# Kernel optimization log

Measured on AMD Instinct MI355X. Metric: run time of the kernel, lower is better.

Reference implementation:

```python
import jax, jax.numpy as jnp
import numpy as np

DIM = 768
NUM_HEADS = 12
HEAD_DIM = DIM // NUM_HEADS
SCALE = HEAD_DIM ** -0.5


def setup_inputs() -> dict:
    key = jax.random.key(0)
    k1, k2, k3, k4 = jax.random.split(key, 4)
    B, N, C = 4, 2048, DIM
    x = jax.random.normal(k1, (B, N, C), dtype=jnp.float32)
    # nn.Linear(dim, 3*dim, bias=False): weight shape (3C, C), y = x @ W^T
    w_qkv = jax.random.normal(k2, (3 * C, C), dtype=jnp.float32) * (C ** -0.5)
    # nn.Linear(dim, dim) with default bias=True
    w_proj = jax.random.normal(k3, (C, C), dtype=jnp.float32) * (C ** -0.5)
    b_proj = jax.random.normal(k4, (C,), dtype=jnp.float32) * 0.02
    return {"x": x, "w_qkv": w_qkv, "w_proj": w_proj, "b_proj": b_proj}


def reference(x, w_qkv, w_proj, b_proj):
    B, N, C = x.shape
    H, D = NUM_HEADS, HEAD_DIM
    qkv = jnp.einsum('bnc,oc->bno', x, w_qkv)  # (B, N, 3C)
    qkv = qkv.reshape(B, N, 3, H, D).transpose(2, 0, 3, 1, 4)  # (3, B, H, N, D)
    q, k, v = qkv[0], qkv[1], qkv[2]
    attn = jnp.einsum('bhnd,bhmd->bhnm', q, k) * jnp.float32(SCALE)  # (B,H,N,N)
    attn = jax.nn.softmax(attn, axis=-1)
    out = jnp.einsum('bhnm,bhmd->bhnd', attn, v)  # (B,H,N,D)
    out = out.transpose(0, 2, 1, 3).reshape(B, N, C)
    out = jnp.einsum('bnc,oc->bno', out, w_proj) + b_proj
    return out
```

## Files before the change

kernel.cpp:

```cpp
#include <hip/hip_runtime.h>
#include <math.h>

#define B_ 4
#define N_ 2048
#define C_ 768
#define H_ 12
#define D_ 64
#define QKSCALE_ 0.18033688011112042f

typedef unsigned short u16;
typedef unsigned int u32;
typedef short s16x8 __attribute__((ext_vector_type(8)));
typedef float f32x4 __attribute__((ext_vector_type(4)));
typedef u32 u32x2 __attribute__((ext_vector_type(2)));

__device__ __forceinline__ u16 f2bf(float f) {
    union { float f; u32 u; } v; v.f = f;
    u32 r = (v.u + 0x7fffu + ((v.u >> 16) & 1u)) >> 16;
    return (u16)r;
}

#if __has_builtin(__builtin_amdgcn_cvt_pk_bf16_f32)
__device__ __forceinline__ u32 pkbf(float a, float b) {
    auto r = __builtin_amdgcn_cvt_pk_bf16_f32(a, b);
    u32 u; __builtin_memcpy(&u, &r, 4);
    return u;
}
#else
__device__ __forceinline__ u32 pkbf(float a, float b) {
    union { float f; u32 u; } ua, ub; ua.f = a; ub.f = b;
    u32 ra = ua.u + 0x7fffu + ((ua.u >> 16) & 1u);
    u32 rb = ub.u + 0x7fffu + ((ub.u >> 16) & 1u);
    return __builtin_amdgcn_perm(rb, ra, 0x07060302u);
}
#endif

__device__ __forceinline__ void gl_lds16(const u16* g, u16* l) {
    __builtin_amdgcn_global_load_lds(
        (__attribute__((address_space(1))) void*)g,
        (__attribute__((address_space(3))) void*)l, 16, 0, 0);
}

#define NX4_  (B_ * N_ * C_ / 4)
#define NWQ4_ (3 * C_ * C_ / 4)
#define NWP4_ (C_ * C_ / 4)
__global__ __launch_bounds__(256) void cvt_all(const float4* __restrict__ x,
                                               const float4* __restrict__ wq,
                                               const float4* __restrict__ wp,
                                               ushort4* __restrict__ xb,
                                               ushort4* __restrict__ wqb,
                                               ushort4* __restrict__ wpb)
{
    const int tot = NX4_ + NWQ4_ + NWP4_;
    int i = blockIdx.x * blockDim.x + threadIdx.x;
    const int stride = gridDim.x * blockDim.x;
    for (; i < tot; i += stride) {
        const float4* s; ushort4* d; int j;
        if (i < NX4_)              { s = x;  d = xb;  j = i; }
        else if (i < NX4_ + NWQ4_) { s = wq; d = wqb; j = i - NX4_; }
        else                       { s = wp; d = wpb; j = i - NX4_ - NWQ4_; }
        float4 v = s[j];
        ushort4 o;
        o.x = f2bf(v.x); o.y = f2bf(v.y); o.z = f2bf(v.z); o.w = f2bf(v.w);
        d[j] = o;
    }
}

template<int BM, bool OUT_BF16, bool BIAS, bool QSCALE>
__global__ __launch_bounds__(256) void gemm_mfma(const u16* __restrict__ A,
                                                 const u16* __restrict__ Bm,
                                                 const float* __restrict__ bias,
                                                 void* __restrict__ Cout,
                                                 int M, int N, int K)
{
    constexpr int MF = BM / 32;
    constexpr int ASZ = BM * 32, BSZ = 128 * 32;
    __shared__ __align__(16) u16 As[2 * ASZ];
    __shared__ __align__(16) u16 Bs[2 * BSZ];
    const int tid  = threadIdx.x;
    const int wv   = tid >> 6;
    const int lane = tid & 63;
    const int lr   = lane & 15;
    const int lq   = lane >> 4;
    const int wm   = (wv >> 1) * (BM / 2);
    const int wn   = (wv & 1) * 64;
    const int row0 = blockIdx.y * BM, col0 = blockIdx.x * 128;

    f32x4 acc[MF][4];
    #pragma unroll
    for (int i = 0; i < MF; i++)
        #pragma unroll
        for (int j = 0; j < 4; j++) { f32x4 z = {0.f,0.f,0.f,0.f}; acc[i][j] = z; }

    const int srow   = lane >> 2;
    const int schunk = (((lane & 3) ^ ((lane >> 3) & 3)) * 8);

    const int arow_base = (BM == 128) ? 32 * wv : 16 * wv;
    const u16* gA0 = A + (size_t)(row0 + arow_base + srow) * K + schunk;
    const u16* gA1 = gA0 + (size_t)16 * K;
    const u16* gB0 = Bm + (size_t)(col0 + 32 * wv + srow) * K + schunk;
    const u16* gB1 = gB0 + (size_t)16 * K;
    const int aoff0 = arow_base * 32, aoff1 = aoff0 + 16 * 32;
    const int boff0 = (32 * wv) * 32, boff1 = boff0 + 16 * 32;

    const int ppos = (lq ^ ((lr >> 1) & 3)) * 8;
    const int nIter = K / 32;

    gl_lds16(gA0, As + aoff0);
    if (BM == 128) gl_lds16(gA1, As + aoff1);
    gl_lds16(gB0, Bs + boff0);
    gl_lds16(gB1, Bs + boff1);

    for (int t = 0; t < nIter; t++) {
        const int cur = t & 1;
        __syncthreads();
        if (t + 1 < nIter) {
            const int k1 = (t + 1) * 32;
            const int nb = cur ^ 1;
            gl_lds16(gA0 + k1, As + nb * ASZ + aoff0);
            if (BM == 128) gl_lds16(gA1 + k1, As + nb * ASZ + aoff1);
            gl_lds16(gB0 + k1, Bs + nb * BSZ + boff0);
            gl_lds16(gB1 + k1, Bs + nb * BSZ + boff1);
        }
        const u16* __restrict__ Ac = As + cur * ASZ;
        const u16* __restrict__ Bc = Bs + cur * BSZ;
        s16x8 af[MF], bfr[4];
        #pragma unroll
        for (int i = 0; i < MF; i++)
            af[i] = *(const s16x8*)&Ac[(wm + 16*i + lr) * 32 + ppos];
        #pragma unroll
        for (int j = 0; j < 4; j++)
            bfr[j] = *(const s16x8*)&Bc[(wn + 16*j + lr) * 32 + ppos];
        #pragma unroll
        for (int i = 0; i < MF; i++)
            #pragma unroll
            for (int j = 0; j < 4; j++)
                acc[i][j] = __builtin_amdgcn_mfma_f32_16x16x32_bf16(af[i], bfr[j], acc[i][j], 0, 0, 0);
    }

    #pragma unroll
    for (int i = 0; i < MF; i++) {
        #pragma unroll
        for (int j = 0; j < 4; j++) {
            const int col = col0 + wn + 16*j + lr;
            float bv = BIAS ? bias[col] : 0.f;
            #pragma unroll
            for (int r = 0; r < 4; r++) {
                const int row = row0 + wm + 16*i + lq*4 + r;
                float v = acc[i][j][r] + bv;
                if (QSCALE && col < C_) v *= QKSCALE_;
                if (OUT_BF16) ((u16*)Cout)[(size_t)row * N + col] = f2bf(v);
                else          ((float*)Cout)[(size_t)row * N + col] = v;
            }
        }
    }
}

__global__ __launch_bounds__(256, 3) void attn_mfma(const u16* __restrict__ qkv,
                                                    u16* __restrict__ attout)
{
    __shared__ __align__(16) u16 Ks[64][72];
    __shared__ __align__(16) u16 Vt[64][72];
    __shared__ __align__(16) u16 Ps[128][72];

    const int tid  = threadIdx.x;
    const int wv   = tid >> 6;
    const int lane = tid & 63;
    const int lr   = lane & 15;
    const int lq   = lane >> 4;
    const int n0   = blockIdx.x * 128;
    const int bh   = blockIdx.y, b = bh / H_, h = bh % H_;
    const size_t rs = 3 * C_;

    const u16* Qg = qkv + ((size_t)b * N_ + n0) * rs + h * D_;
    const u16* Kg = qkv + ((size_t)b * N_) * rs + C_ + h * D_;
    const u16* Vg = Kg + C_;

    s16x8 qf[2][2];
    #pragma unroll
    for (int iq = 0; iq < 2; iq++)
        #pragma unroll
        for (int kk = 0; kk < 2; kk++)
            qf[iq][kk] = *(const s16x8*)(Qg + (size_t)(32*wv + 16*iq + lr) * rs + kk*32 + lq*8);

    f32x4 oacc[2][4];
    float li[2] = {0.f, 0.f};
    #pragma unroll
    for (int i = 0; i < 2; i++)
        #pragma unroll
        for (int j = 0; j < 4; j++) { f32x4 z = {0.f,0.f,0.f,0.f}; oacc[i][j] = z; }

    const int skey = tid >> 2, sd0 = (tid & 3) * 16;
    const int vc = tid & 7, vp = tid >> 3;
    const int vkey0 = 2 * vp, vd0 = vc * 8;
    const int vcol0 = (vkey0 + 8 * vc) & 63;

    s16x8 kr0, kr1, vr0, vr1;
    {
        const u16* kp = Kg + (size_t)skey * rs + sd0;
        kr0 = *(const s16x8*)kp; kr1 = *(const s16x8*)(kp + 8);
        const u16* vp2 = Vg + (size_t)vkey0 * rs + vd0;
        vr0 = *(const s16x8*)vp2; vr1 = *(const s16x8*)(vp2 + rs);
    }

    for (int t = 0; t < N_ / 64; t++) {
        __syncthreads();
        *(s16x8*)&Ks[skey][sd0]     = kr0;
        *(s16x8*)&Ks[skey][sd0 + 8] = kr1;
        #pragma unroll
        for (int u = 0; u < 8; u++) {
            u32 pk = (u32)(u16)vr0[u] | ((u32)(u16)vr1[u] << 16);
            *(u32*)&Vt[vd0 + u][vcol0] = pk;
        }
        __syncthreads();
        if (t + 1 < N_ / 64) {
            const u16* kp = Kg + (size_t)((t+1)*64 + skey) * rs + sd0;
            kr0 = *(const s16x8*)kp; kr1 = *(const s16x8*)(kp + 8);
            const u16* vp2 = Vg + (size_t)((t+1)*64 + vkey0) * rs + vd0;
            vr0 = *(const s16x8*)vp2; vr1 = *(const s16x8*)(vp2 + rs);
        }

        f32x4 st[4][2];
        #pragma unroll
        for (int jk = 0; jk < 4; jk++)
            #pragma unroll
            for (int iq = 0; iq < 2; iq++) { f32x4 z = {0.f,0.f,0.f,0.f}; st[jk][iq] = z; }
        #pragma unroll
        for (int kk = 0; kk < 2; kk++) {
            s16x8 kf[4];
            #pragma unroll
            for (int jk = 0; jk < 4; jk++)
                kf[jk] = *(const s16x8*)&Ks[16*jk + lr][kk*32 + lq*8];
            #pragma unroll
            for (int jk = 0; jk < 4; jk++) {
                st[jk][0] = __builtin_amdgcn_mfma_f32_16x16x32_bf16(kf[jk], qf[0][kk], st[jk][0], 0, 0, 0);
                st[jk][1] = __builtin_amdgcn_mfma_f32_16x16x32_bf16(kf[jk], qf[1][kk], st[jk][1], 0, 0, 0);
            }
        }

        #pragma unroll
        for (int jk = 0; jk < 4; jk++)
            #pragma unroll
            for (int iq = 0; iq < 2; iq++) {
                const float p0 = __builtin_amdgcn_exp2f(st[jk][iq][0]);
                const float p1 = __builtin_amdgcn_exp2f(st[jk][iq][1]);
                const float p2 = __builtin_amdgcn_exp2f(st[jk][iq][2]);
                const float p3 = __builtin_amdgcn_exp2f(st[jk][iq][3]);
                li[iq] += (p0 + p1) + (p2 + p3);
                u32x2 w;
                w.x = pkbf(p0, p1);
                w.y = pkbf(p2, p3);
                *(u32x2*)&Ps[32*wv + 16*iq + lr][16*jk + 4*lq] = w;
            }

        #pragma unroll
        for (int kk = 0; kk < 2; kk++) {
            s16x8 ap0 = *(const s16x8*)&Ps[32*wv      + lr][kk*32 + lq*8];
            s16x8 ap1 = *(const s16x8*)&Ps[32*wv + 16 + lr][kk*32 + lq*8];
            #pragma unroll
            for (int j2 = 0; j2 < 4; j2++) {
                const int pb = ((kk*4 + lq) + 2*j2 + (lr >> 3)) & 7;
                s16x8 bv = *(const s16x8*)&Vt[16*j2 + lr][pb * 8];
                oacc[0][j2] = __builtin_amdgcn_mfma_f32_16x16x32_bf16(ap0, bv, oacc[0][j2], 0, 0, 0);
                oacc[1][j2] = __builtin_amdgcn_mfma_f32_16x16x32_bf16(ap1, bv, oacc[1][j2], 0, 0, 0);
            }
        }
    }

    #pragma unroll
    for (int iq = 0; iq < 2; iq++) {
        li[iq] += __shfl_xor(li[iq], 16);
        li[iq] += __shfl_xor(li[iq], 32);
    }
    #pragma unroll
    for (int iq = 0; iq < 2; iq++) {
        #pragma unroll
        for (int r = 0; r < 4; r++) {
            const float inv = 1.f / __shfl(li[iq], 4*lq + r);
            const int row = n0 + 32*wv + 16*iq + 4*lq + r;
            #pragma unroll
            for (int j2 = 0; j2 < 4; j2++)
                attout[((size_t)(b * N_ + row)) * C_ + h * D_ + 16*j2 + lr] =
                    f2bf(oacc[iq][j2][r] * inv);
        }
    }
}

extern "C" void kernel_launch(void* const* d_in, const int* in_sizes, int n_in,
                              void* d_out, int out_size, void* d_ws, size_t ws_size,
                              hipStream_t stream) {
    const float* x      = (const float*)d_in[0];
    const float* w_qkv  = (const float*)d_in[1];
    const float* w_proj = (const float*)d_in[2];
    const float* b_proj = (const float*)d_in[3];
    float* out = (float*)d_out;

    const int NX   = B_ * N_ * C_;
    const int NWQ  = 3 * C_ * C_;
    const int NWP  = C_ * C_;
    const int NQKV = B_ * N_ * 3 * C_;

    u16* xb   = (u16*)d_ws;
    u16* wqb  = xb + NX;
    u16* wpb  = wqb + NWQ;
    u16* qkvb = wpb + NWP;
    u16* attb = qkvb + NQKV;

    dim3 blk(256);

    cvt_all<<<768, blk, 0, stream>>>((const float4*)x, (const float4*)w_qkv,
                                     (const float4*)w_proj,
                                     (ushort4*)xb, (ushort4*)wqb, (ushort4*)wpb);

    const int M = B_ * N_;
    gemm_mfma<128, true, false, true><<<dim3((3*C_)/128, M/128), blk, 0, stream>>>(
        xb, wqb, nullptr, qkvb, M, 3*C_, C_);

    attn_mfma<<<dim3(N_/128, B_ * H_), blk, 0, stream>>>(qkvb, attb);

    gemm_mfma<64, false, true, false><<<dim3(C_/128, M/64), blk, 0, stream>>>(
        attb, wpb, b_proj, out, M, C_, C_);
}
```

Before: 227.5 us.

## Enlarge QKV GEMM tile, swizzle attention LDS, raise occupancy bounds

New measurement: 241.8 us. +6.3%, slower.

```diff
diff --git a/kernel.cpp b/kernel.cpp
--- a/kernel.cpp
+++ b/kernel.cpp
@@ -20,20 +20,12 @@
     return (u16)r;
 }
 
-#if __has_builtin(__builtin_amdgcn_cvt_pk_bf16_f32)
-__device__ __forceinline__ u32 pkbf(float a, float b) {
-    auto r = __builtin_amdgcn_cvt_pk_bf16_f32(a, b);
-    u32 u; __builtin_memcpy(&u, &r, 4);
-    return u;
-}
-#else
 __device__ __forceinline__ u32 pkbf(float a, float b) {
     union { float f; u32 u; } ua, ub; ua.f = a; ub.f = b;
     u32 ra = ua.u + 0x7fffu + ((ua.u >> 16) & 1u);
     u32 rb = ub.u + 0x7fffu + ((ub.u >> 16) & 1u);
     return __builtin_amdgcn_perm(rb, ra, 0x07060302u);
 }
-#endif
 
 __device__ __forceinline__ void gl_lds16(const u16* g, u16* l) {
     __builtin_amdgcn_global_load_lds(
@@ -66,14 +58,15 @@
     }
 }
 
-template<int BM, bool OUT_BF16, bool BIAS, bool QSCALE>
-__global__ __launch_bounds__(256) void gemm_mfma(const u16* __restrict__ A,
-                                                 const u16* __restrict__ Bm,
-                                                 const float* __restrict__ bias,
-                                                 void* __restrict__ Cout,
-                                                 int M, int N, int K)
+template<int BM, int WPEU, bool OUT_BF16, bool BIAS, bool QSCALE>
+__global__ __launch_bounds__(256, WPEU) void gemm_mfma(const u16* __restrict__ A,
+                                                       const u16* __restrict__ Bm,
+                                                       const float* __restrict__ bias,
+                                                       void* __restrict__ Cout,
+                                                       int M, int N, int K)
 {
     constexpr int MF = BM / 32;
+    constexpr int ACALLS = BM / 64;
     constexpr int ASZ = BM * 32, BSZ = 128 * 32;
     __shared__ __align__(16) u16 As[2 * ASZ];
     __shared__ __align__(16) u16 Bs[2 * BSZ];
@@ -95,19 +88,19 @@
     const int srow   = lane >> 2;
     const int schunk = (((lane & 3) ^ ((lane >> 3) & 3)) * 8);
 
-    const int arow_base = (BM == 128) ? 32 * wv : 16 * wv;
+    const int arow_base = (BM / 4) * wv;
     const u16* gA0 = A + (size_t)(row0 + arow_base + srow) * K + schunk;
-    const u16* gA1 = gA0 + (size_t)16 * K;
     const u16* gB0 = Bm + (size_t)(col0 + 32 * wv + srow) * K + schunk;
     const u16* gB1 = gB0 + (size_t)16 * K;
-    const int aoff0 = arow_base * 32, aoff1 = aoff0 + 16 * 32;
+    const int aoff0 = arow_base * 32;
     const int boff0 = (32 * wv) * 32, boff1 = boff0 + 16 * 32;
 
     const int ppos = (lq ^ ((lr >> 1) & 3)) * 8;
     const int nIter = K / 32;
 
-    gl_lds16(gA0, As + aoff0);
-    if (BM == 128) gl_lds16(gA1, As + aoff1);
+    #pragma unroll
+    for (int c = 0; c < ACALLS; c++)
+        gl_lds16(gA0 + (size_t)(16 * c) * K, As + aoff0 + c * 16 * 32);
     gl_lds16(gB0, Bs + boff0);
     gl_lds16(gB1, Bs + boff1);
 
@@ -117,8 +110,10 @@
         if (t + 1 < nIter) {
             const int k1 = (t + 1) * 32;
             const int nb = cur ^ 1;
-            gl_lds16(gA0 + k1, As + nb * ASZ + aoff0);
-            if (BM == 128) gl_lds16(gA1 + k1, As + nb * ASZ + aoff1);
+            #pragma unroll
+            for (int c = 0; c < ACALLS; c++)
+                gl_lds16(gA0 + (size_t)(16 * c) * K + k1,
+                         As + nb * ASZ + aoff0 + c * 16 * 32);
             gl_lds16(gB0 + k1, Bs + nb * BSZ + boff0);
             gl_lds16(gB1 + k1, Bs + nb * BSZ + boff1);
         }
@@ -156,12 +151,12 @@
     }
 }
 
-__global__ __launch_bounds__(256, 3) void attn_mfma(const u16* __restrict__ qkv,
+__global__ __launch_bounds__(256, 4) void attn_mfma(const u16* __restrict__ qkv,
                                                     u16* __restrict__ attout)
 {
-    __shared__ __align__(16) u16 Ks[64][72];
+    __shared__ __align__(16) u16 Ks[64 * 64];
     __shared__ __align__(16) u16 Vt[64][72];
-    __shared__ __align__(16) u16 Ps[128][72];
+    __shared__ __align__(16) u16 Ps[128 * 64];
 
     const int tid  = threadIdx.x;
     const int wv   = tid >> 6;
@@ -190,14 +185,17 @@
         #pragma unroll
         for (int j = 0; j < 4; j++) { f32x4 z = {0.f,0.f,0.f,0.f}; oacc[i][j] = z; }
 
-    const int skey = tid >> 2, sd0 = (tid & 3) * 16;
+    const int skey = tid >> 2;
+    const int sc0  = (tid & 3) * 2;
+    const int scA  = (sc0     ^ (skey & 7)) * 8;
+    const int scB  = ((sc0+1) ^ (skey & 7)) * 8;
     const int vc = tid & 7, vp = tid >> 3;
     const int vkey0 = 2 * vp, vd0 = vc * 8;
     const int vcol0 = (vkey0 + 8 * vc) & 63;
 
     s16x8 kr0, kr1, vr0, vr1;
     {
-        const u16* kp = Kg + (size_t)skey * rs + sd0;
+        const u16* kp = Kg + (size_t)skey * rs + sc0 * 8;
         kr0 = *(const s16x8*)kp; kr1 = *(const s16x8*)(kp + 8);
         const u16* vp2 = Vg + (size_t)vkey0 * rs + vd0;
         vr0 = *(const s16x8*)vp2; vr1 = *(const s16x8*)(vp2 + rs);
@@ -205,8 +203,8 @@
 
     for (int t = 0; t < N_ / 64; t++) {
         __syncthreads();
-        *(s16x8*)&Ks[skey][sd0]     = kr0;
-        *(s16x8*)&Ks[skey][sd0 + 8] = kr1;
+        *(s16x8*)&Ks[skey * 64 + scA] = kr0;
+        *(s16x8*)&Ks[skey * 64 + scB] = kr1;
         #pragma unroll
         for (int u = 0; u < 8; u++) {
             u32 pk = (u32)(u16)vr0[u] | ((u32)(u16)vr1[u] << 16);
@@ -214,7 +212,7 @@
         }
         __syncthreads();
         if (t + 1 < N_ / 64) {
-            const u16* kp = Kg + (size_t)((t+1)*64 + skey) * rs + sd0;
+            const u16* kp = Kg + (size_t)((t+1)*64 + skey) * rs + sc0 * 8;
             kr0 = *(const s16x8*)kp; kr1 = *(const s16x8*)(kp + 8);
             const u16* vp2 = Vg + (size_t)((t+1)*64 + vkey0) * rs + vd0;
             vr0 = *(const s16x8*)vp2; vr1 = *(const s16x8*)(vp2 + rs);
@@ -230,7 +228,7 @@
             s16x8 kf[4];
             #pragma unroll
             for (int jk = 0; jk < 4; jk++)
-                kf[jk] = *(const s16x8*)&Ks[16*jk + lr][kk*32 + lq*8];
+                kf[jk] = *(const s16x8*)&Ks[(16*jk + lr) * 64 + ((4*kk + lq) ^ (lr & 7)) * 8];
             #pragma unroll
             for (int jk = 0; jk < 4; jk++) {
                 st[jk][0] = __builtin_amdgcn_mfma_f32_16x16x32_bf16(kf[jk], qf[0][kk], st[jk][0], 0, 0, 0);
@@ -250,13 +248,15 @@
                 u32x2 w;
                 w.x = pkbf(p0, p1);
                 w.y = pkbf(p2, p3);
-                *(u32x2*)&Ps[32*wv + 16*iq + lr][16*jk + 4*lq] = w;
+                const int prow = 32*wv + 16*iq + lr;
+                const int pch  = ((2*jk + (lq >> 1)) ^ (lr & 7)) * 8 + (lq & 1) * 4;
+                *(u32x2*)&Ps[prow * 64 + pch] = w;
             }
 
         #pragma unroll
         for (int kk = 0; kk < 2; kk++) {
-            s16x8 ap0 = *(const s16x8*)&Ps[32*wv      + lr][kk*32 + lq*8];
-            s16x8 ap1 = *(const s16x8*)&Ps[32*wv + 16 + lr][kk*32 + lq*8];
+            s16x8 ap0 = *(const s16x8*)&Ps[(32*wv      + lr) * 64 + ((4*kk + lq) ^ (lr & 7)) * 8];
+            s16x8 ap1 = *(const s16x8*)&Ps[(32*wv + 16 + lr) * 64 + ((4*kk + lq) ^ (lr & 7)) * 8];
             #pragma unroll
             for (int j2 = 0; j2 < 4; j2++) {
                 const int pb = ((kk*4 + lq) + 2*j2 + (lr >> 3)) & 7;
@@ -313,11 +313,11 @@
                                      (ushort4*)xb, (ushort4*)wqb, (ushort4*)wpb);
 
     const int M = B_ * N_;
-    gemm_mfma<128, true, false, true><<<dim3((3*C_)/128, M/128), blk, 0, stream>>>(
+    gemm_mfma<256, 2, true, false, true><<<dim3((3*C_)/128, M/256), blk, 0, stream>>>(
         xb, wqb, nullptr, qkvb, M, 3*C_, C_);
 
     attn_mfma<<<dim3(N_/128, B_ * H_), blk, 0, stream>>>(qkvb, attb);
 
-    gemm_mfma<64, false, true, false><<<dim3(C_/128, M/64), blk, 0, stream>>>(
+    gemm_mfma<64, 4, false, true, false><<<dim3(C_/128, M/64), blk, 0, stream>>>(
         attb, wpb, b_proj, out, M, C_, C_);
 }
```
